# Kernel tuning notes

Measured on AMD Instinct MI355X. Metric: run time of the kernel, lower is better.

## Reference

```python
import math
import jax, jax.numpy as jnp
import numpy as np

B, T, N = 64, 100, 20
NR = N * (N - 1)
D_STATE, D_SHAPE, D_REL = 8, 4, 3
THRESH = 0.35


def _pair_indices(n):
    # (i, j) pairs with i != j, ordered so that relation index
    # r = i*(n-1) + j - (j > i) equals the flattened position.
    ii, jj = np.meshgrid(np.arange(n), np.arange(n), indexing='ij')
    m = ii != jj
    return ii[m], jj[m]  # each [n*(n-1)]


def setup_inputs() -> dict:
    key = jax.random.key(0)
    k1, k2, k3 = jax.random.split(key, 3)
    objects_state = jax.random.uniform(k1, (B, T, N, D_STATE), dtype=jnp.float32)
    objects_shape = jax.random.normal(k2, (B, T, N, D_SHAPE), dtype=jnp.float32)
    relation_info = jax.random.normal(k3, (B, T, NR, D_REL), dtype=jnp.float32)
    return {"objects_state": objects_state, "objects_shape": objects_shape,
            "relation_info": relation_info}


def reference(objects_state, objects_shape, relation_info):
    dt = objects_state.dtype
    i_idx, j_idx = _pair_indices(N)

    # cdist over xy positions, then threshold (diagonal is exactly 0 -> excluded by nonzero)
    pos = objects_state[..., 0:2]                                   # [B,T,N,2]
    d = jnp.linalg.norm(pos[..., :, None, :] - pos[..., None, :, :], axis=-1)  # [B,T,N,N]
    adj = (d < THRESH) & (d > 0)
    mask = adj[..., i_idx, j_idx].astype(dt)                        # [B,T,NR]

    eye = jnp.eye(N, dtype=dt)
    receiver_relations = mask[..., None] * eye[i_idx]               # [B,T,NR,N]
    sender_relations = mask[..., None] * eye[j_idx]                 # [B,T,NR,N]

    # identity scaler
    data_state, data_shape = objects_state, objects_shape

    senders_state = jnp.einsum('btrn,btnd->btrd', sender_relations, data_state)
    receivers_state = jnp.einsum('btrn,btnd->btrd', receiver_relations, data_state)
    senders_shape = jnp.einsum('btrn,btnd->btrd', sender_relations, data_shape)
    receivers_shape = jnp.einsum('btrn,btnd->btrd', receiver_relations, data_shape)

    recv_ang = receivers_state[..., 2:3]                            # [B,T,NR,1]
    half_pi = jnp.asarray(math.pi / 2, dtype=dt)
    b1 = jnp.concatenate([jnp.cos(recv_ang), jnp.sin(recv_ang)], axis=-1)
    b2 = jnp.concatenate([jnp.cos(recv_ang + half_pi), jnp.sin(recv_ang + half_pi)], axis=-1)
    basis = jnp.stack([b1, b2], axis=-2)                            # [B,T,NR,2,2]

    diff_state = senders_state - receivers_state
    diff_pos = diff_state[..., 0:2]
    diff_vel = diff_state[..., 3:5]
    control = senders_state[..., 6:8]
    angle_diff = diff_state[..., 2:3]
    angle_diff_vel = diff_state[..., 5:6]

    temp = jnp.stack([diff_pos, diff_vel, control], axis=-1)        # [B,T,NR,2,3]
    tfed = jnp.einsum('btrij,btrjk->btrik', basis, temp)            # [B,T,NR,2,3]
    diff_pos, diff_vel, control = tfed[..., 0], tfed[..., 1], tfed[..., 2]

    diff_angle_2d = jnp.concatenate([jnp.sin(2 * angle_diff), jnp.cos(2 * angle_diff)], axis=-1)
    diff_state = jnp.concatenate([diff_pos, diff_vel, control, diff_angle_2d, angle_diff_vel], axis=-1)
    rel_data = jnp.concatenate([relation_info, diff_state, receivers_shape, senders_shape], axis=-1)

    obj_ang = data_state[..., 2:3]                                  # [B,T,N,1]
    ob1 = jnp.concatenate([jnp.cos(obj_ang), jnp.sin(obj_ang)], axis=-1)
    ob2 = jnp.concatenate([jnp.cos(obj_ang + half_pi), jnp.sin(obj_ang + half_pi)], axis=-1)
    object_basis = jnp.stack([ob1, ob2], axis=-2)                   # [B,T,N,2,2]
    obj_vel = data_state[..., 3:5]
    obj_vel_tfed = jnp.einsum('btnij,btnj->btni', object_basis, obj_vel)
    obj_data = jnp.concatenate([obj_vel_tfed, data_state[..., 5:6], data_shape], axis=-1)

    return rel_data, obj_data, receiver_relations, sender_relations
```

## Files before the change

### kernel.cpp

```cpp
#include <hip/hip_runtime.h>
#include <math.h>

#define BB 64
#define TT 100
#define NN 20
#define NRR 380

typedef float f32x4 __attribute__((ext_vector_type(4)));

__device__ __forceinline__ void compute_row(
    int r, float ri0, float ri1, float ri2,
    const float* __restrict__ s_state, const float* __restrict__ s_shape,
    float4* __restrict__ s_row4, float* __restrict__ s_mask, int* __restrict__ s_ij)
{
    const float THRESH  = 0.35f;
    const float HALF_PI = 1.57079632679489661923f;

    const int i = r / 19;
    const int l = r - i * 19;
    const int j = (l < i) ? l : (l + 1);

    const float* si = &s_state[i * 8];
    const float* sj = &s_state[j * 8];

    const float dx = si[0] - sj[0];
    const float dy = si[1] - sj[1];
    const float d  = sqrtf(dx * dx + dy * dy);
    const float mask = (d < THRESH && d > 0.0f) ? 1.0f : 0.0f;

    const float dpx   = mask * (sj[0] - si[0]);
    const float dpy   = mask * (sj[1] - si[1]);
    const float adiff = mask * (sj[2] - si[2]);
    const float dvx   = mask * (sj[3] - si[3]);
    const float dvy   = mask * (sj[4] - si[4]);
    const float adv   = mask * (sj[5] - si[5]);
    const float cx    = mask * sj[6];
    const float cy    = mask * sj[7];

    const float rang = mask * si[2];
    const float c1 = cosf(rang),           s1 = sinf(rang);
    const float c2 = cosf(rang + HALF_PI), s2 = sinf(rang + HALF_PI);

    float4 w0, w1, w2, w3, w4;
    w0.x = ri0; w0.y = ri1; w0.z = ri2;
    w0.w = c1 * dpx + s1 * dpy;
    w1.x = c2 * dpx + s2 * dpy;
    w1.y = c1 * dvx + s1 * dvy;
    w1.z = c2 * dvx + s2 * dvy;
    w1.w = c1 * cx  + s1 * cy;
    w2.x = c2 * cx  + s2 * cy;
    w2.y = sinf(2.0f * adiff);
    w2.z = cosf(2.0f * adiff);
    w2.w = adv;
    w3.x = mask * s_shape[i * 4 + 0];
    w3.y = mask * s_shape[i * 4 + 1];
    w3.z = mask * s_shape[i * 4 + 2];
    w3.w = mask * s_shape[i * 4 + 3];
    w4.x = mask * s_shape[j * 4 + 0];
    w4.y = mask * s_shape[j * 4 + 1];
    w4.z = mask * s_shape[j * 4 + 2];
    w4.w = mask * s_shape[j * 4 + 3];

    float4* row = &s_row4[r * 5];
    row[0] = w0; row[1] = w1; row[2] = w2; row[3] = w3; row[4] = w4;
    s_mask[r] = mask;
    s_ij[r]   = i | (j << 8);
}

__global__ __launch_bounds__(256) void gp_kernel(
    const float* __restrict__ state,
    const float* __restrict__ shape,
    const float* __restrict__ relinfo,
    float* __restrict__ out)
{
    const int bt  = blockIdx.x;
    const int tid = threadIdx.x;

    __shared__ float  s_state[NN * 8];
    __shared__ float  s_shape[NN * 4];
    __shared__ float4 s_row4[NRR * 5];
    __shared__ float  s_mask[NRR];
    __shared__ int    s_ij[NRR];

    const int   r2v   = tid + 256;
    const int   r2c   = (r2v < NRR) ? r2v : (NRR - 1);
    const float* rbase = relinfo + (size_t)bt * NRR * 3;
    const float ra0 = rbase[tid * 3 + 0];
    const float ra1 = rbase[tid * 3 + 1];
    const float ra2 = rbase[tid * 3 + 2];
    const float rb0 = rbase[r2c * 3 + 0];
    const float rb1 = rbase[r2c * 3 + 1];
    const float rb2 = rbase[r2c * 3 + 2];

    if (tid < NN * 8)                   s_state[tid]          = state[(size_t)bt * NN * 8 + tid];
    else if (tid < NN * 8 + NN * 4)     s_shape[tid - NN * 8] = shape[(size_t)bt * NN * 4 + (tid - NN * 8)];
    __syncthreads();

    const size_t REL_SZ = (size_t)BB * TT * NRR * 20;
    const size_t OBJ_SZ = (size_t)BB * TT * NN * 7;
    f32x4* relb  = (f32x4*)out                              + (size_t)bt * (NRR * 5);
    float* objb  = out + REL_SZ                             + (size_t)bt * (NN * 7);
    f32x4* recvb = (f32x4*)(out + REL_SZ + OBJ_SZ)          + (size_t)bt * (NRR * 5);
    f32x4* sendb = (f32x4*)(out + REL_SZ + OBJ_SZ + REL_SZ) + (size_t)bt * (NRR * 5);

    if (tid < NN * 7) {
        const float HALF_PI = 1.57079632679489661923f;
        const int n = tid / 7;
        const int c = tid - n * 7;
        float v;
        if (c < 2) {
            const float ang = s_state[n * 8 + 2];
            const float a   = (c == 0) ? ang : (ang + HALF_PI);
            v = cosf(a) * s_state[n * 8 + 3] + sinf(a) * s_state[n * 8 + 4];
        } else if (c == 2) {
            v = s_state[n * 8 + 5];
        } else {
            v = s_shape[n * 4 + (c - 3)];
        }
        objb[tid] = v;
    }

    compute_row(tid, ra0, ra1, ra2, s_state, s_shape, s_row4, s_mask, s_ij);
    if (r2v < NRR)
        compute_row(r2v, rb0, rb1, rb2, s_state, s_shape, s_row4, s_mask, s_ij);
    __syncthreads();

    float4 w[8];
    float  m[8];
    int    ij[8];
#pragma unroll
    for (int k = 0; k < 8; ++k) {
        const int idx  = tid + k * 256;
        const int idxc = (idx < NRR * 5) ? idx : 0;
        w[k]  = s_row4[idxc];
        m[k]  = s_mask[idxc / 5];
        ij[k] = s_ij[idxc / 5];
    }
#pragma unroll
    for (int k = 0; k < 8; ++k) {
        const int idx = tid + k * 256;
        if (idx < NRR * 5) {
            const int r  = idx / 5;
            const int qb = (idx - r * 5) * 4;
            const int i  = ij[k] & 255;
            const int j  = ij[k] >> 8;
            f32x4 wv, rv, sv;
            wv.x = w[k].x; wv.y = w[k].y; wv.z = w[k].z; wv.w = w[k].w;
            rv.x = (i == qb + 0) ? m[k] : 0.0f;
            rv.y = (i == qb + 1) ? m[k] : 0.0f;
            rv.z = (i == qb + 2) ? m[k] : 0.0f;
            rv.w = (i == qb + 3) ? m[k] : 0.0f;
            sv.x = (j == qb + 0) ? m[k] : 0.0f;
            sv.y = (j == qb + 1) ? m[k] : 0.0f;
            sv.z = (j == qb + 2) ? m[k] : 0.0f;
            sv.w = (j == qb + 3) ? m[k] : 0.0f;
            __builtin_nontemporal_store(wv, &relb[idx]);
            __builtin_nontemporal_store(rv, &recvb[idx]);
            __builtin_nontemporal_store(sv, &sendb[idx]);
        }
    }
}

extern "C" void kernel_launch(void* const* d_in, const int* in_sizes, int n_in,
                              void* d_out, int out_size, void* d_ws, size_t ws_size,
                              hipStream_t stream) {
    const float* state = (const float*)d_in[0];
    const float* shp   = (const float*)d_in[1];
    const float* rel   = (const float*)d_in[2];
    float* out = (float*)d_out;
    gp_kernel<<<dim3(BB * TT), dim3(256), 0, stream>>>(state, shp, rel, out);
}
```

Before: 125.1 us.

## Split fused kernel into rel-data kernel and one-hot relation kernel

Splits the single fused kernel into two launches. One computes rel_data and obj_data, and the other recomputes the mask and writes the receiver and sender one-hot matrices. The aim is to lower per-kernel register and shared-memory pressure and to simplify each store loop. In exchange it adds a second launch, reloads positions and recomputes the distance mask, and loses the interleaving of the three output streams within one block.

```diff
diff --git a/kernel.cpp b/kernel.cpp
--- a/kernel.cpp
+++ b/kernel.cpp
@@ -8,66 +8,76 @@
 
 typedef float f32x4 __attribute__((ext_vector_type(4)));
 
-__device__ __forceinline__ void compute_row(
-    int r, float ri0, float ri1, float ri2,
-    const float* __restrict__ s_state, const float* __restrict__ s_shape,
-    float4* __restrict__ s_row4, float* __restrict__ s_mask, int* __restrict__ s_ij)
+__global__ __launch_bounds__(256) void onehot_kernel(
+    const float* __restrict__ state,
+    float* __restrict__ out)
 {
-    const float THRESH  = 0.35f;
-    const float HALF_PI = 1.57079632679489661923f;
-
-    const int i = r / 19;
-    const int l = r - i * 19;
-    const int j = (l < i) ? l : (l + 1);
-
-    const float* si = &s_state[i * 8];
-    const float* sj = &s_state[j * 8];
-
-    const float dx = si[0] - sj[0];
-    const float dy = si[1] - sj[1];
-    const float d  = sqrtf(dx * dx + dy * dy);
-    const float mask = (d < THRESH && d > 0.0f) ? 1.0f : 0.0f;
-
-    const float dpx   = mask * (sj[0] - si[0]);
-    const float dpy   = mask * (sj[1] - si[1]);
-    const float adiff = mask * (sj[2] - si[2]);
-    const float dvx   = mask * (sj[3] - si[3]);
-    const float dvy   = mask * (sj[4] - si[4]);
-    const float adv   = mask * (sj[5] - si[5]);
-    const float cx    = mask * sj[6];
-    const float cy    = mask * sj[7];
-
-    const float rang = mask * si[2];
-    const float c1 = cosf(rang),           s1 = sinf(rang);
-    const float c2 = cosf(rang + HALF_PI), s2 = sinf(rang + HALF_PI);
-
-    float4 w0, w1, w2, w3, w4;
-    w0.x = ri0; w0.y = ri1; w0.z = ri2;
-    w0.w = c1 * dpx + s1 * dpy;
-    w1.x = c2 * dpx + s2 * dpy;
-    w1.y = c1 * dvx + s1 * dvy;
-    w1.z = c2 * dvx + s2 * dvy;
-    w1.w = c1 * cx  + s1 * cy;
-    w2.x = c2 * cx  + s2 * cy;
-    w2.y = sinf(2.0f * adiff);
-    w2.z = cosf(2.0f * adiff);
-    w2.w = adv;
-    w3.x = mask * s_shape[i * 4 + 0];
-    w3.y = mask * s_shape[i * 4 + 1];
-    w3.z = mask * s_shape[i * 4 + 2];
-    w3.w = mask * s_shape[i * 4 + 3];
-    w4.x = mask * s_shape[j * 4 + 0];
-    w4.y = mask * s_shape[j * 4 + 1];
-    w4.z = mask * s_shape[j * 4 + 2];
-    w4.w = mask * s_shape[j * 4 + 3];
-
-    float4* row = &s_row4[r * 5];
-    row[0] = w0; row[1] = w1; row[2] = w2; row[3] = w3; row[4] = w4;
-    s_mask[r] = mask;
-    s_ij[r]   = i | (j << 8);
+    const int bt  = blockIdx.x;
+    const int tid = threadIdx.x;
+
+    __shared__ float s_pos[NN * 2];
+    __shared__ float s_mask[NRR];
+    __shared__ int   s_ij[NRR];
+
+    if (tid < NN * 2) {
+        const int n = tid >> 1, c = tid & 1;
+        s_pos[tid] = state[(size_t)bt * NN * 8 + n * 8 + c];
+    }
+    __syncthreads();
+
+    const float THRESH = 0.35f;
+    for (int r = tid; r < NRR; r += 256) {
+        const int i = r / 19;
+        const int l = r - i * 19;
+        const int j = (l < i) ? l : (l + 1);
+        const float dx = s_pos[i * 2 + 0] - s_pos[j * 2 + 0];
+        const float dy = s_pos[i * 2 + 1] - s_pos[j * 2 + 1];
+        const float d  = sqrtf(dx * dx + dy * dy);
+        s_mask[r] = (d < THRESH && d > 0.0f) ? 1.0f : 0.0f;
+        s_ij[r]   = i | (j << 8);
+    }
+    __syncthreads();
+
+    const size_t REL_SZ = (size_t)BB * TT * NRR * 20;
+    const size_t OBJ_SZ = (size_t)BB * TT * NN * 7;
+    f32x4* recvb = (f32x4*)(out + REL_SZ + OBJ_SZ)          + (size_t)bt * (NRR * 5);
+    f32x4* sendb = (f32x4*)(out + REL_SZ + OBJ_SZ + REL_SZ) + (size_t)bt * (NRR * 5);
+
+#pragma unroll
+    for (int k = 0; k < 8; ++k) {
+        const int idx = tid + k * 256;
+        if (idx < NRR * 5) {
+            const int r  = idx / 5;
+            const int qb = (idx - r * 5) * 4;
+            const float m = s_mask[r];
+            const int   i = s_ij[r] & 255;
+            f32x4 rv;
+            rv.x = (i == qb + 0) ? m : 0.0f;
+            rv.y = (i == qb + 1) ? m : 0.0f;
+            rv.z = (i == qb + 2) ? m : 0.0f;
+            rv.w = (i == qb + 3) ? m : 0.0f;
+            __builtin_nontemporal_store(rv, &recvb[idx]);
+        }
+    }
+#pragma unroll
+    for (int k = 0; k < 8; ++k) {
+        const int idx = tid + k * 256;
+        if (idx < NRR * 5) {
+            const int r  = idx / 5;
+            const int qb = (idx - r * 5) * 4;
+            const float m = s_mask[r];
+            const int   j = s_ij[r] >> 8;
+            f32x4 sv;
+            sv.x = (j == qb + 0) ? m : 0.0f;
+            sv.y = (j == qb + 1) ? m : 0.0f;
+            sv.z = (j == qb + 2) ? m : 0.0f;
+            sv.w = (j == qb + 3) ? m : 0.0f;
+            __builtin_nontemporal_store(sv, &sendb[idx]);
+        }
+    }
 }
 
-__global__ __launch_bounds__(256) void gp_kernel(
+__global__ __launch_bounds__(256) void reldata_kernel(
     const float* __restrict__ state,
     const float* __restrict__ shape,
     const float* __restrict__ relinfo,
@@ -79,11 +89,12 @@
     __shared__ float  s_state[NN * 8];
     __shared__ float  s_shape[NN * 4];
     __shared__ float4 s_row4[NRR * 5];
-    __shared__ float  s_mask[NRR];
-    __shared__ int    s_ij[NRR];
-
-    const int   r2v   = tid + 256;
-    const int   r2c   = (r2v < NRR) ? r2v : (NRR - 1);
+
+    const float THRESH  = 0.35f;
+    const float HALF_PI = 1.57079632679489661923f;
+
+    const int   r2v = tid + 256;
+    const int   r2c = (r2v < NRR) ? r2v : (NRR - 1);
     const float* rbase = relinfo + (size_t)bt * NRR * 3;
     const float ra0 = rbase[tid * 3 + 0];
     const float ra1 = rbase[tid * 3 + 1];
@@ -97,14 +108,10 @@
     __syncthreads();
 
     const size_t REL_SZ = (size_t)BB * TT * NRR * 20;
-    const size_t OBJ_SZ = (size_t)BB * TT * NN * 7;
-    f32x4* relb  = (f32x4*)out                              + (size_t)bt * (NRR * 5);
-    float* objb  = out + REL_SZ                             + (size_t)bt * (NN * 7);
-    f32x4* recvb = (f32x4*)(out + REL_SZ + OBJ_SZ)          + (size_t)bt * (NRR * 5);
-    f32x4* sendb = (f32x4*)(out + REL_SZ + OBJ_SZ + REL_SZ) + (size_t)bt * (NRR * 5);
+    f32x4* relb = (f32x4*)out + (size_t)bt * (NRR * 5);
+    float* objb = out + REL_SZ + (size_t)bt * (NN * 7);
 
     if (tid < NN * 7) {
-        const float HALF_PI = 1.57079632679489661923f;
         const int n = tid / 7;
         const int c = tid - n * 7;
         float v;
@@ -120,43 +127,72 @@
         objb[tid] = v;
     }
 
-    compute_row(tid, ra0, ra1, ra2, s_state, s_shape, s_row4, s_mask, s_ij);
-    if (r2v < NRR)
-        compute_row(r2v, rb0, rb1, rb2, s_state, s_shape, s_row4, s_mask, s_ij);
-    __syncthreads();
-
-    float4 w[8];
-    float  m[8];
-    int    ij[8];
-#pragma unroll
-    for (int k = 0; k < 8; ++k) {
-        const int idx  = tid + k * 256;
-        const int idxc = (idx < NRR * 5) ? idx : 0;
-        w[k]  = s_row4[idxc];
-        m[k]  = s_mask[idxc / 5];
-        ij[k] = s_ij[idxc / 5];
-    }
+    for (int pass = 0; pass < 2; ++pass) {
+        const int r = (pass == 0) ? tid : r2v;
+        if (r < NRR) {
+            const float f0 = (pass == 0) ? ra0 : rb0;
+            const float f1 = (pass == 0) ? ra1 : rb1;
+            const float f2 = (pass == 0) ? ra2 : rb2;
+
+            const int i = r / 19;
+            const int l = r - i * 19;
+            const int j = (l < i) ? l : (l + 1);
+
+            const float* si = &s_state[i * 8];
+            const float* sj = &s_state[j * 8];
+
+            const float dx = si[0] - sj[0];
+            const float dy = si[1] - sj[1];
+            const float d  = sqrtf(dx * dx + dy * dy);
+            const float mask = (d < THRESH && d > 0.0f) ? 1.0f : 0.0f;
+
+            const float dpx   = mask * (sj[0] - si[0]);
+            const float dpy   = mask * (sj[1] - si[1]);
+            const float adiff = mask * (sj[2] - si[2]);
+            const float dvx   = mask * (sj[3] - si[3]);
+            const float dvy   = mask * (sj[4] - si[4]);
+            const float adv   = mask * (sj[5] - si[5]);
+            const float cx    = mask * sj[6];
+            const float cy    = mask * sj[7];
+
+            const float rang = mask * si[2];
+            const float c1 = cosf(rang),           s1 = sinf(rang);
+            const float c2 = cosf(rang + HALF_PI), s2 = sinf(rang + HALF_PI);
+
+            float4 w0, w1, w2, w3, w4;
+            w0.x = f0; w0.y = f1; w0.z = f2;
+            w0.w = c1 * dpx + s1 * dpy;
+            w1.x = c2 * dpx + s2 * dpy;
+            w1.y = c1 * dvx + s1 * dvy;
+            w1.z = c2 * dvx + s2 * dvy;
+            w1.w = c1 * cx  + s1 * cy;
+            w2.x = c2 * cx  + s2 * cy;
+            w2.y = sinf(2.0f * adiff);
+            w2.z = cosf(2.0f * adiff);
+            w2.w = adv;
+            w3.x = mask * s_shape[i * 4 + 0];
+            w3.y = mask * s_shape[i * 4 + 1];
+            w3.z = mask * s_shape[i * 4 + 2];
+            w3.w = mask * s_shape[i * 4 + 3];
+            w4.x = mask * s_shape[j * 4 + 0];
+            w4.y = mask * s_shape[j * 4 + 1];
+            w4.z = mask * s_shape[j * 4 + 2];
+            w4.w = mask * s_shape[j * 4 + 3];
+
+            float4* row = &s_row4[r * 5];
+            row[0] = w0; row[1] = w1; row[2] = w2; row[3] = w3; row[4] = w4;
+        }
+    }
+    __syncthreads();
+
 #pragma unroll
     for (int k = 0; k < 8; ++k) {
         const int idx = tid + k * 256;
         if (idx < NRR * 5) {
-            const int r  = idx / 5;
-            const int qb = (idx - r * 5) * 4;
-            const int i  = ij[k] & 255;
-            const int j  = ij[k] >> 8;
-            f32x4 wv, rv, sv;
-            wv.x = w[k].x; wv.y = w[k].y; wv.z = w[k].z; wv.w = w[k].w;
-            rv.x = (i == qb + 0) ? m[k] : 0.0f;
-            rv.y = (i == qb + 1) ? m[k] : 0.0f;
-            rv.z = (i == qb + 2) ? m[k] : 0.0f;
-            rv.w = (i == qb + 3) ? m[k] : 0.0f;
-            sv.x = (j == qb + 0) ? m[k] : 0.0f;
-            sv.y = (j == qb + 1) ? m[k] : 0.0f;
-            sv.z = (j == qb + 2) ? m[k] : 0.0f;
-            sv.w = (j == qb + 3) ? m[k] : 0.0f;
+            const float4 w = s_row4[idx];
+            f32x4 wv;
+            wv.x = w.x; wv.y = w.y; wv.z = w.z; wv.w = w.w;
             __builtin_nontemporal_store(wv, &relb[idx]);
-            __builtin_nontemporal_store(rv, &recvb[idx]);
-            __builtin_nontemporal_store(sv, &sendb[idx]);
         }
     }
 }
@@ -168,5 +204,6 @@
     const float* shp   = (const float*)d_in[1];
     const float* rel   = (const float*)d_in[2];
     float* out = (float*)d_out;
-    gp_kernel<<<dim3(BB * TT), dim3(256), 0, stream>>>(state, shp, rel, out);
+    reldata_kernel<<<dim3(BB * TT), dim3(256), 0, stream>>>(state, shp, rel, out);
+    onehot_kernel <<<dim3(BB * TT), dim3(256), 0, stream>>>(state, out);
 }
```

After: 120.7 us. 3.5% less time.
